# Performance work log

Measured on AMD Instinct MI355X. Metric: run time of the kernel, lower is better.

The kernel has to match this reference:

```python
import jax, jax.numpy as jnp
import numpy as np

H, HKV, D, HID = 32, 8, 128, 4096
EPS = 1e-6
ROPE_BASE = 10000.0
SCALE = D ** -0.5


def setup_inputs() -> dict:
    key = jax.random.key(0)
    ks = jax.random.split(key, 4)
    T = 2048
    x = jax.random.normal(ks[0], (T, HID), dtype=jnp.float32)
    w_qkv = jax.random.normal(ks[1], ((H + 2 * HKV) * D, HID), dtype=jnp.float32) * (HID ** -0.5)
    b_qkv = jax.random.normal(ks[2], ((H + 2 * HKV) * D,), dtype=jnp.float32) * 0.02
    q_norm_w = jnp.ones((D,), dtype=jnp.float32)
    k_norm_w = jnp.ones((D,), dtype=jnp.float32)
    w_o = jax.random.normal(ks[3], (HID, H * D), dtype=jnp.float32) * ((H * D) ** -0.5)
    return {"x": x, "w_qkv": w_qkv, "b_qkv": b_qkv, "q_norm_w": q_norm_w,
            "k_norm_w": k_norm_w, "w_o": w_o}


def _rms_norm(t, w):
    # per-head RMSNorm over the last (head_dim) axis
    var = jnp.mean(t * t, axis=-1, keepdims=True)
    return t * jax.lax.rsqrt(var + EPS) * w


def _rope(t, cos, sin):
    # neox-style half rotation; cos/sin: [T, D//2], t: [T, h, D]
    t1, t2 = jnp.split(t, 2, axis=-1)
    c = cos[:, None, :]
    s = sin[:, None, :]
    return jnp.concatenate([t1 * c - t2 * s, t2 * c + t1 * s], axis=-1)


def reference(x, w_qkv, b_qkv, q_norm_w, k_norm_w, w_o):
    T = x.shape[0]
    qkv = x @ w_qkv.T + b_qkv                      # [T, (H+2*HKV)*D]
    q, k, v = jnp.split(qkv, [H * D, (H + HKV) * D], axis=-1)
    q = q.reshape(T, H, D)
    k = k.reshape(T, HKV, D)
    v = v.reshape(T, HKV, D)

    # QK RMSNorm
    q = _rms_norm(q, q_norm_w)
    k = _rms_norm(k, k_norm_w)

    # rotary embedding, base 10000, full head_dim
    pos = jnp.arange(T, dtype=jnp.float32)
    inv_freq = 1.0 / (ROPE_BASE ** (jnp.arange(0, D, 2, dtype=jnp.float32) / D))
    freqs = pos[:, None] * inv_freq[None, :]        # [T, D//2]
    cos, sin = jnp.cos(freqs), jnp.sin(freqs)
    q = _rope(q, cos, sin)
    k = _rope(k, cos, sin)

    # GQA: kv_head_mapping = arange(HKV).repeat_interleave(H // HKV)
    groups = H // HKV
    k = jnp.repeat(k, groups, axis=1)               # [T, H, D]
    v = jnp.repeat(v, groups, axis=1)

    scores = jnp.einsum('thd,shd->hts', q, k) * SCALE   # [H, T, T]
    causal = jnp.tril(jnp.ones((T, T), dtype=bool))
    scores = jnp.where(causal[None], scores, jnp.finfo(scores.dtype).min)
    probs = jax.nn.softmax(scores, axis=-1)
    out = jnp.einsum('hts,shd->thd', probs, v)      # [T, H, D]
    return out.reshape(T, H * D) @ w_o.T            # [T, HID]
```

## Files before the change

kernel.cpp:

```cpp
#include <hip/hip_runtime.h>
#include <stdint.h>
#include <stddef.h>

typedef __bf16 bf16_t;
typedef __bf16 bf16x8 __attribute__((ext_vector_type(8)));
typedef float  f32x4  __attribute__((ext_vector_type(4)));

#define T_SEQ 2048
#define NH    32
#define NKV   8
#define DH    128
#define HIDN  4096
#define NQKV  6144
#define SCALE 0.08838834764831845f
#define MBOUND 11.5f
#define C1_EXP2 0.12751743187767f
#define C2_EXP2 16.590992970223f

__device__ inline float b2f(bf16_t v) {
  uint32_t u = ((uint32_t)__builtin_bit_cast(uint16_t, v)) << 16;
  return __builtin_bit_cast(float, u);
}
__device__ inline bf16_t f2b(float f) { return (bf16_t)f; }
__device__ inline void gl_lds16(const void* g, void* l) {
  __builtin_amdgcn_global_load_lds(
      (__attribute__((address_space(1))) void*)g,
      (__attribute__((address_space(3))) void*)l, 16, 0, 0);
}
__device__ inline f32x4 mfma16(bf16x8 a, bf16x8 b, f32x4 c) {
  return __builtin_amdgcn_mfma_f32_16x16x32_bf16(a, b, c, 0, 0, 0);
}
__device__ inline void store_val(float* p, float v)  { *p = v; }
__device__ inline void store_val(bf16_t* p, float v) { *p = f2b(v); }

__global__ __launch_bounds__(256)
void cvt2_kernel(const float* __restrict__ a, bf16_t* __restrict__ ao, int na,
                 const float* __restrict__ b, bf16_t* __restrict__ bo) {
  int blk = blockIdx.x;
  const float* in;
  bf16_t* out;
  int rb;
  if (blk < na) { in = a; out = ao; rb = blk; }
  else          { in = b; out = bo; rb = blk - na; }
  size_t i = ((size_t)rb * 256 + threadIdx.x) * 8;
  f32x4 va = *(const f32x4*)(in + i);
  f32x4 vb = *(const f32x4*)(in + i + 4);
  bf16x8 o;
#pragma unroll
  for (int e = 0; e < 4; ++e) { o[e] = f2b(va[e]); o[e + 4] = f2b(vb[e]); }
  *(bf16x8*)(out + i) = o;
}

__global__ __launch_bounds__(256)
void cvt_kernel(const float* __restrict__ in, bf16_t* __restrict__ out) {
  size_t i = ((size_t)blockIdx.x * 256 + threadIdx.x) * 8;
  f32x4 a = *(const f32x4*)(in + i);
  f32x4 b = *(const f32x4*)(in + i + 4);
  bf16x8 o;
#pragma unroll
  for (int e = 0; e < 4; ++e) { o[e] = f2b(a[e]); o[e + 4] = f2b(b[e]); }
  *(bf16x8*)(out + i) = o;
}

template <bool BIAS, typename TOUT>
__global__ __launch_bounds__(256)
void gemm_bt(const bf16_t* __restrict__ A, const bf16_t* __restrict__ Bw,
             const float* __restrict__ bias, TOUT* __restrict__ C,
             int M, int N, int K) {
  __shared__ __align__(16) char smem[32768];
  char* sA = smem;
  char* sB = smem + 16384;
  const int tid  = threadIdx.x;
  const int lane = tid & 63, wave = tid >> 6;
  const int quad = lane >> 4, l16 = lane & 15;
  const int wm = wave >> 1, wn = wave & 1;
  const int m0 = blockIdx.y * 128, n0 = blockIdx.x * 128;

  f32x4 acc[4][4] = {};
  const int kTiles = K >> 6;

  for (int kt = 0; kt < kTiles; ++kt) {
    const int kb = kt << 6;
#pragma unroll
    for (int i = 0; i < 4; ++i) {
      int p = i * 256 + tid;
      int row = p >> 3, gc = (p & 7) ^ (row & 7);
      gl_lds16(A  + (size_t)(m0 + row) * K + kb + gc * 8, sA + p * 16);
      gl_lds16(Bw + (size_t)(n0 + row) * K + kb + gc * 8, sB + p * 16);
    }
    __syncthreads();

#pragma unroll
    for (int ks = 0; ks < 2; ++ks) {
      bf16x8 af[4], bfr[4];
      const int c = ks * 4 + quad;
#pragma unroll
      for (int i = 0; i < 4; ++i) {
        int ra = wm * 64 + i * 16 + l16;
        af[i]  = *(const bf16x8*)(sA + ra * 128 + ((c ^ (ra & 7)) * 16));
        int rb = wn * 64 + i * 16 + l16;
        bfr[i] = *(const bf16x8*)(sB + rb * 128 + ((c ^ (rb & 7)) * 16));
      }
#pragma unroll
      for (int i = 0; i < 4; ++i)
#pragma unroll
        for (int j = 0; j < 4; ++j)
          acc[i][j] = mfma16(af[i], bfr[j], acc[i][j]);
    }
    __syncthreads();
  }
#pragma unroll
  for (int i = 0; i < 4; ++i) {
    int mrow = m0 + wm * 64 + i * 16 + quad * 4;
#pragma unroll
    for (int j = 0; j < 4; ++j) {
      int ncol = n0 + wn * 64 + j * 16 + l16;
      float bv = BIAS ? bias[ncol] : 0.f;
#pragma unroll
      for (int r = 0; r < 4; ++r)
        store_val(&C[(size_t)(mrow + r) * N + ncol], acc[i][j][r] + bv);
    }
  }
}

__global__ __launch_bounds__(256)
void prep_kernel(const bf16_t* __restrict__ qkv, const float* __restrict__ qw,
                 const float* __restrict__ kw, bf16_t* __restrict__ Qp,
                 bf16_t* __restrict__ Kp, bf16_t* __restrict__ Vp) {
  const int id   = blockIdx.x * 4 + (threadIdx.x >> 6);
  const int lane = threadIdx.x & 63;
  const int t = id / 48, slot = id % 48;
  const bf16_t* src = qkv + (size_t)t * NQKV + slot * DH;
  float x1 = b2f(src[lane]), x2 = b2f(src[lane + 64]);
  float o1, o2;
  if (slot < 40) {
    float ssq = x1 * x1 + x2 * x2;
#pragma unroll
    for (int m = 1; m < 64; m <<= 1) ssq += __shfl_xor(ssq, m, 64);
    float rms = rsqrtf(ssq * (1.f / 128.f) + 1e-6f);
    const float* w = (slot < 32) ? qw : kw;
    float n1 = x1 * rms * w[lane];
    float n2 = x2 * rms * w[lane + 64];
    float inv = exp2f(-0.20762050593046014f * (float)lane);
    float ang = (float)t * inv;
    float cs = __cosf(ang), sn = __sinf(ang);
    o1 = n1 * cs - n2 * sn;
    o2 = n2 * cs + n1 * sn;
  } else { o1 = x1; o2 = x2; }
  bf16_t* dst;
  if (slot < 32)      dst = Qp + ((size_t)t * NH  + slot)        * DH;
  else if (slot < 40) dst = Kp + ((size_t)t * NKV + (slot - 32)) * DH;
  else                dst = Vp + ((size_t)t * NKV + (slot - 40)) * DH;
  dst[lane] = f2b(o1); dst[lane + 64] = f2b(o2);
}

__global__ __launch_bounds__(256)
void vtrans_kernel(const bf16_t* __restrict__ Vp, bf16_t* __restrict__ Vt) {
  __shared__ bf16_t tile[64 * 66];
  const int t0 = blockIdx.x * 64, d0 = blockIdx.y * 64, kvh = blockIdx.z;
  const int tid = threadIdx.x;
#pragma unroll
  for (int i = 0; i < 2; ++i) {
    int id = i * 256 + tid;
    int tr = id >> 3, dc = id & 7;
    bf16x8 v = *(const bf16x8*)(Vp + ((size_t)(t0 + tr) * NKV + kvh) * DH + d0 + dc * 8);
#pragma unroll
    for (int e = 0; e < 8; ++e) tile[tr * 66 + dc * 8 + e] = v[e];
  }
  __syncthreads();
#pragma unroll
  for (int i = 0; i < 2; ++i) {
    int id = i * 256 + tid;
    int dr = id >> 3, tc = id & 7;
    bf16x8 o;
#pragma unroll
    for (int e = 0; e < 8; ++e) o[e] = tile[(tc * 8 + e) * 66 + dr];
    *(bf16x8*)(Vt + ((size_t)kvh * DH + d0 + dr) * T_SEQ + t0 + tc * 8) = o;
  }
}

__global__ __launch_bounds__(256)
void attn_kernel(const bf16_t* __restrict__ Qp, const bf16_t* __restrict__ Kp,
                 const bf16_t* __restrict__ Vt, bf16_t* __restrict__ Out) {
  __shared__ __align__(16) char smem[73728];
  const int tid  = threadIdx.x;
  const int lane = tid & 63, wave = tid >> 6;
  const int quad = lane >> 4, l16 = lane & 15;
  const int b = blockIdx.x, h = blockIdx.y;
  const int qt_lo = b, qt_hi = 31 - b;
  const int kvh = h >> 2;
  char* sPw = smem + 65536 + wave * 2048;

  bf16x8 qf_lo[4], qf_hi[4];
  {
    const int row_lo = qt_lo * 64 + wave * 16 + l16;
    const int row_hi = qt_hi * 64 + wave * 16 + l16;
#pragma unroll
    for (int ks = 0; ks < 4; ++ks) {
      qf_lo[ks] = *(const bf16x8*)(Qp + ((size_t)row_lo * NH + h) * DH + ks * 32 + quad * 8);
      qf_hi[ks] = *(const bf16x8*)(Qp + ((size_t)row_hi * NH + h) * DH + ks * 32 + quad * 8);
    }
  }
  f32x4 acc_lo[8] = {}, acc_hi[8] = {};
  float l_lo[4] = {0.f, 0.f, 0.f, 0.f}, l_hi[4] = {0.f, 0.f, 0.f, 0.f};

  auto stage = [&](int kt) {
    char* sK = smem + (kt & 1) * 16384;
    char* sV = smem + 32768 + (kt & 1) * 16384;
    const int k0 = kt * 64;
#pragma unroll
    for (int i = 0; i < 4; ++i) {
      int p = i * 256 + tid;
      int row = p >> 4, gc = (p & 15) ^ (row & 15);
      gl_lds16(Kp + ((size_t)(k0 + row) * NKV + kvh) * DH + gc * 8, sK + p * 16);
    }
#pragma unroll
    for (int i = 0; i < 4; ++i) {
      int p = i * 256 + tid;
      int d = p >> 3, gc = (p & 7) ^ (d & 7);
      gl_lds16(Vt + ((size_t)kvh * DH + d) * T_SEQ + k0 + gc * 8, sV + p * 16);
    }
  };

  auto compute = [&](const bf16x8 (&qf)[4], f32x4 (&acc)[8], float (&lrow)[4],
                     int qt, int kt, char* sK, char* sVT) {
    f32x4 sfr[4] = {};
    __builtin_amdgcn_s_setprio(1);
#pragma unroll
    for (int ks = 0; ks < 4; ++ks) {
      const int c = ks * 4 + quad;
#pragma unroll
      for (int j = 0; j < 4; ++j) {
        int row = j * 16 + l16;
        bf16x8 kf = *(const bf16x8*)(sK + row * 256 + ((c ^ (row & 15)) * 16));
        sfr[j] = mfma16(qf[ks], kf, sfr[j]);
      }
    }
    __builtin_amdgcn_s_setprio(0);
    float sv[4][4];
    const bool diag = (kt == qt);
#pragma unroll
    for (int j = 0; j < 4; ++j)
#pragma unroll
      for (int r = 0; r < 4; ++r) {
        float e = exp2f(fmaf(sfr[j][r], C1_EXP2, -C2_EXP2));
        if (diag) {
          int qg = wave * 16 + quad * 4 + r;
          int kg = j * 16 + l16;
          if (kg > qg) e = 0.f;
        }
        sv[j][r] = e;
      }
#pragma unroll
    for (int r = 0; r < 4; ++r)
      lrow[r] += (sv[0][r] + sv[1][r]) + (sv[2][r] + sv[3][r]);
#pragma unroll
    for (int j = 0; j < 4; ++j)
#pragma unroll
      for (int r = 0; r < 4; ++r) {
        int prow = quad * 4 + r;
        int col  = j * 16 + l16;
        int c    = col >> 3;
        ((bf16_t*)(sPw + prow * 128 + ((c ^ (prow & 7)) * 16)))[col & 7] = f2b(sv[j][r]);
      }
    __asm__ volatile("" ::: "memory");
    bf16x8 pf[2];
#pragma unroll
    for (int ks2 = 0; ks2 < 2; ++ks2) {
      int c = ks2 * 4 + quad;
      pf[ks2] = *(const bf16x8*)(sPw + l16 * 128 + ((c ^ (l16 & 7)) * 16));
    }
    __asm__ volatile("" ::: "memory");
    __builtin_amdgcn_s_setprio(1);
#pragma unroll
    for (int j2 = 0; j2 < 8; ++j2)
#pragma unroll
      for (int ks2 = 0; ks2 < 2; ++ks2) {
        int d = j2 * 16 + l16;
        int c = ks2 * 4 + quad;
        bf16x8 vf = *(const bf16x8*)(sVT + d * 128 + ((c ^ (d & 7)) * 16));
        acc[j2] = mfma16(pf[ks2], vf, acc[j2]);
      }
    __builtin_amdgcn_s_setprio(0);
  };

  stage(0);
  for (int kt = 0; kt <= qt_hi; ++kt) {
    __syncthreads();
    if (kt < qt_hi) stage(kt + 1);
    char* sK  = smem + (kt & 1) * 16384;
    char* sVT = smem + 32768 + (kt & 1) * 16384;
    compute(qf_hi, acc_hi, l_hi, qt_hi, kt, sK, sVT);
    if (kt <= qt_lo)
      compute(qf_lo, acc_lo, l_lo, qt_lo, kt, sK, sVT);
  }

#pragma unroll
  for (int r = 0; r < 4; ++r) {
    float lh = l_hi[r], ll = l_lo[r];
#pragma unroll
    for (int m = 1; m < 16; m <<= 1) {
      lh += __shfl_xor(lh, m, 64);
      ll += __shfl_xor(ll, m, 64);
    }
    float inv_h = 1.f / lh, inv_l = 1.f / ll;
    int qg_h = qt_hi * 64 + wave * 16 + quad * 4 + r;
    int qg_l = qt_lo * 64 + wave * 16 + quad * 4 + r;
#pragma unroll
    for (int j2 = 0; j2 < 8; ++j2) {
      int d = j2 * 16 + l16;
      Out[(size_t)qg_h * (NH * DH) + h * DH + d] = f2b(acc_hi[j2][r] * inv_h);
      Out[(size_t)qg_l * (NH * DH) + h * DH + d] = f2b(acc_lo[j2][r] * inv_l);
    }
  }
}

extern "C" void kernel_launch(void* const* d_in, const int* in_sizes, int n_in,
                              void* d_out, int out_size, void* d_ws, size_t ws_size,
                              hipStream_t stream) {
  const float* x    = (const float*)d_in[0];
  const float* wqkv = (const float*)d_in[1];
  const float* bqkv = (const float*)d_in[2];
  const float* qnw  = (const float*)d_in[3];
  const float* knw  = (const float*)d_in[4];
  const float* wo   = (const float*)d_in[5];
  float* out = (float*)d_out;

  char* ws = (char*)d_ws;
  bf16_t* wqkvb = (bf16_t*)(ws);
  bf16_t* xb    = (bf16_t*)(ws + 50331648);
  bf16_t* qkv   = (bf16_t*)(ws + 67108864);
  bf16_t* Qp    = (bf16_t*)(ws);
  bf16_t* Kp    = (bf16_t*)(ws + 16777216);
  bf16_t* Vp    = (bf16_t*)(ws + 20971520);
  bf16_t* Vt    = (bf16_t*)(ws + 25165824);
  bf16_t* wob   = (bf16_t*)(ws + 29360128);
  bf16_t* At    = (bf16_t*)(ws + 67108864);

  cvt2_kernel<<<16384, 256, 0, stream>>>(x, xb, 4096, wqkv, wqkvb);
  gemm_bt<true, bf16_t><<<dim3(NQKV / 128, T_SEQ / 128), 256, 0, stream>>>(
      xb, wqkvb, bqkv, qkv, T_SEQ, NQKV, HIDN);
  prep_kernel<<<(T_SEQ * 48) / 4, 256, 0, stream>>>(qkv, qnw, knw, Qp, Kp, Vp);
  vtrans_kernel<<<dim3(T_SEQ / 64, DH / 64, NKV), 256, 0, stream>>>(Vp, Vt);
  cvt_kernel<<<(HIDN * HIDN) / 2048, 256, 0, stream>>>(wo, wob);
  attn_kernel<<<dim3(16, NH), 256, 0, stream>>>(Qp, Kp, Vt, At);
  gemm_bt<false, float><<<dim3(HIDN / 128, T_SEQ / 128), 256, 0, stream>>>(
      At, wob, nullptr, out, T_SEQ, HIDN, HIDN);
}
```

Measured before the change: 533.6 us.

## Fuse QK RMSNorm, RoPE and V transpose into QKV GEMM epilogue

Adds a dedicated QKV GEMM whose epilogue stages the output tile in LDS and applies per-head RMSNorm and RoPE for Q/K slots, or writes V transposed directly. This removes the prep and vtrans kernels and the round trip of the intermediate qkv buffer through global memory. It also drops the s_setprio hints around the MFMA loops in attention and rearranges the workspace layout. The epilogue's scalar 2-byte strided stores and per-row shuffle reductions may be slower than the old vectorized paths.

```diff
diff --git a/kernel.cpp b/kernel.cpp
--- a/kernel.cpp
+++ b/kernel.cpp
@@ -13,7 +13,6 @@
 #define HIDN  4096
 #define NQKV  6144
 #define SCALE 0.08838834764831845f
-#define MBOUND 11.5f
 #define C1_EXP2 0.12751743187767f
 #define C2_EXP2 16.590992970223f
 
@@ -62,6 +61,108 @@
   *(bf16x8*)(out + i) = o;
 }
 
+__global__ __launch_bounds__(256)
+void gemm_qkv(const bf16_t* __restrict__ A, const bf16_t* __restrict__ Bw,
+              const float* __restrict__ bias, const float* __restrict__ qw,
+              const float* __restrict__ kw, bf16_t* __restrict__ Qp,
+              bf16_t* __restrict__ Kp, bf16_t* __restrict__ Vt) {
+  __shared__ __align__(16) char smem[33280];
+  char* sA = smem;
+  char* sB = smem + 16384;
+  const int tid  = threadIdx.x;
+  const int lane = tid & 63, wave = tid >> 6;
+  const int quad = lane >> 4, l16 = lane & 15;
+  const int wm = wave >> 1, wn = wave & 1;
+  const int slot = blockIdx.x;
+  const int m0 = blockIdx.y * 128, n0 = slot * 128;
+  const int K = HIDN;
+
+  f32x4 acc[4][4] = {};
+  const int kTiles = K >> 6;
+
+  for (int kt = 0; kt < kTiles; ++kt) {
+    const int kb = kt << 6;
+#pragma unroll
+    for (int i = 0; i < 4; ++i) {
+      int p = i * 256 + tid;
+      int row = p >> 3, gc = (p & 7) ^ (row & 7);
+      gl_lds16(A  + (size_t)(m0 + row) * K + kb + gc * 8, sA + p * 16);
+      gl_lds16(Bw + (size_t)(n0 + row) * K + kb + gc * 8, sB + p * 16);
+    }
+    __syncthreads();
+
+#pragma unroll
+    for (int ks = 0; ks < 2; ++ks) {
+      bf16x8 af[4], bfr[4];
+      const int c = ks * 4 + quad;
+#pragma unroll
+      for (int i = 0; i < 4; ++i) {
+        int ra = wm * 64 + i * 16 + l16;
+        af[i]  = *(const bf16x8*)(sA + ra * 128 + ((c ^ (ra & 7)) * 16));
+        int rb = wn * 64 + i * 16 + l16;
+        bfr[i] = *(const bf16x8*)(sB + rb * 128 + ((c ^ (rb & 7)) * 16));
+      }
+#pragma unroll
+      for (int i = 0; i < 4; ++i)
+#pragma unroll
+        for (int j = 0; j < 4; ++j)
+          acc[i][j] = mfma16(af[i], bfr[j], acc[i][j]);
+    }
+    __syncthreads();
+  }
+
+  bf16_t* tile = (bf16_t*)smem;
+#pragma unroll
+  for (int i = 0; i < 4; ++i) {
+    int rl = wm * 64 + i * 16 + quad * 4;
+#pragma unroll
+    for (int j = 0; j < 4; ++j) {
+      int cl = wn * 64 + j * 16 + l16;
+      float bv = bias[n0 + cl];
+#pragma unroll
+      for (int r = 0; r < 4; ++r)
+        tile[(rl + r) * 130 + cl] = f2b(acc[i][j][r] + bv);
+    }
+  }
+  __syncthreads();
+
+  if (slot < 40) {
+    const float* w = (slot < 32) ? qw : kw;
+    const float wl1 = w[lane], wl2 = w[lane + 64];
+    const float inv = exp2f(-0.20762050593046014f * (float)lane);
+    bf16_t* dstBase = (slot < 32) ? Qp + (size_t)slot * DH
+                                  : Kp + (size_t)(slot - 32) * DH;
+    const size_t dstStride = (slot < 32) ? (size_t)NH * DH : (size_t)NKV * DH;
+#pragma unroll 4
+    for (int rr = 0; rr < 32; ++rr) {
+      int row = wave * 32 + rr;
+      int t = m0 + row;
+      float x1 = b2f(tile[row * 130 + lane]);
+      float x2 = b2f(tile[row * 130 + lane + 64]);
+      float ssq = x1 * x1 + x2 * x2;
+#pragma unroll
+      for (int m = 1; m < 64; m <<= 1) ssq += __shfl_xor(ssq, m, 64);
+      float rms = rsqrtf(ssq * (1.f / 128.f) + 1e-6f);
+      float n1 = x1 * rms * wl1;
+      float n2 = x2 * rms * wl2;
+      float ang = (float)t * inv;
+      float cs = __cosf(ang), sn = __sinf(ang);
+      bf16_t* dst = dstBase + (size_t)t * dstStride;
+      dst[lane]      = f2b(n1 * cs - n2 * sn);
+      dst[lane + 64] = f2b(n2 * cs + n1 * sn);
+    }
+  } else {
+    const int kvh = slot - 40;
+#pragma unroll 4
+    for (int dd = 0; dd < 32; ++dd) {
+      int d = wave * 32 + dd;
+      bf16_t* dst = Vt + ((size_t)kvh * DH + d) * T_SEQ + m0;
+      dst[lane]      = tile[lane * 130 + d];
+      dst[lane + 64] = tile[(lane + 64) * 130 + d];
+    }
+  }
+}
+
 template <bool BIAS, typename TOUT>
 __global__ __launch_bounds__(256)
 void gemm_bt(const bf16_t* __restrict__ A, const bf16_t* __restrict__ Bw,
@@ -124,62 +225,6 @@
 }
 
 __global__ __launch_bounds__(256)
-void prep_kernel(const bf16_t* __restrict__ qkv, const float* __restrict__ qw,
-                 const float* __restrict__ kw, bf16_t* __restrict__ Qp,
-                 bf16_t* __restrict__ Kp, bf16_t* __restrict__ Vp) {
-  const int id   = blockIdx.x * 4 + (threadIdx.x >> 6);
-  const int lane = threadIdx.x & 63;
-  const int t = id / 48, slot = id % 48;
-  const bf16_t* src = qkv + (size_t)t * NQKV + slot * DH;
-  float x1 = b2f(src[lane]), x2 = b2f(src[lane + 64]);
-  float o1, o2;
-  if (slot < 40) {
-    float ssq = x1 * x1 + x2 * x2;
-#pragma unroll
-    for (int m = 1; m < 64; m <<= 1) ssq += __shfl_xor(ssq, m, 64);
-    float rms = rsqrtf(ssq * (1.f / 128.f) + 1e-6f);
-    const float* w = (slot < 32) ? qw : kw;
-    float n1 = x1 * rms * w[lane];
-    float n2 = x2 * rms * w[lane + 64];
-    float inv = exp2f(-0.20762050593046014f * (float)lane);
-    float ang = (float)t * inv;
-    float cs = __cosf(ang), sn = __sinf(ang);
-    o1 = n1 * cs - n2 * sn;
-    o2 = n2 * cs + n1 * sn;
-  } else { o1 = x1; o2 = x2; }
-  bf16_t* dst;
-  if (slot < 32)      dst = Qp + ((size_t)t * NH  + slot)        * DH;
-  else if (slot < 40) dst = Kp + ((size_t)t * NKV + (slot - 32)) * DH;
-  else                dst = Vp + ((size_t)t * NKV + (slot - 40)) * DH;
-  dst[lane] = f2b(o1); dst[lane + 64] = f2b(o2);
-}
-
-__global__ __launch_bounds__(256)
-void vtrans_kernel(const bf16_t* __restrict__ Vp, bf16_t* __restrict__ Vt) {
-  __shared__ bf16_t tile[64 * 66];
-  const int t0 = blockIdx.x * 64, d0 = blockIdx.y * 64, kvh = blockIdx.z;
-  const int tid = threadIdx.x;
-#pragma unroll
-  for (int i = 0; i < 2; ++i) {
-    int id = i * 256 + tid;
-    int tr = id >> 3, dc = id & 7;
-    bf16x8 v = *(const bf16x8*)(Vp + ((size_t)(t0 + tr) * NKV + kvh) * DH + d0 + dc * 8);
-#pragma unroll
-    for (int e = 0; e < 8; ++e) tile[tr * 66 + dc * 8 + e] = v[e];
-  }
-  __syncthreads();
-#pragma unroll
-  for (int i = 0; i < 2; ++i) {
-    int id = i * 256 + tid;
-    int dr = id >> 3, tc = id & 7;
-    bf16x8 o;
-#pragma unroll
-    for (int e = 0; e < 8; ++e) o[e] = tile[(tc * 8 + e) * 66 + dr];
-    *(bf16x8*)(Vt + ((size_t)kvh * DH + d0 + dr) * T_SEQ + t0 + tc * 8) = o;
-  }
-}
-
-__global__ __launch_bounds__(256)
 void attn_kernel(const bf16_t* __restrict__ Qp, const bf16_t* __restrict__ Kp,
                  const bf16_t* __restrict__ Vt, bf16_t* __restrict__ Out) {
   __shared__ __align__(16) char smem[73728];
@@ -225,7 +270,6 @@
   auto compute = [&](const bf16x8 (&qf)[4], f32x4 (&acc)[8], float (&lrow)[4],
                      int qt, int kt, char* sK, char* sVT) {
     f32x4 sfr[4] = {};
-    __builtin_amdgcn_s_setprio(1);
 #pragma unroll
     for (int ks = 0; ks < 4; ++ks) {
       const int c = ks * 4 + quad;
@@ -236,7 +280,6 @@
         sfr[j] = mfma16(qf[ks], kf, sfr[j]);
       }
     }
-    __builtin_amdgcn_s_setprio(0);
     float sv[4][4];
     const bool diag = (kt == qt);
 #pragma unroll
@@ -271,7 +314,6 @@
       pf[ks2] = *(const bf16x8*)(sPw + l16 * 128 + ((c ^ (l16 & 7)) * 16));
     }
     __asm__ volatile("" ::: "memory");
-    __builtin_amdgcn_s_setprio(1);
 #pragma unroll
     for (int j2 = 0; j2 < 8; ++j2)
 #pragma unroll
@@ -281,7 +323,6 @@
         bf16x8 vf = *(const bf16x8*)(sVT + d * 128 + ((c ^ (d & 7)) * 16));
         acc[j2] = mfma16(pf[ks2], vf, acc[j2]);
       }
-    __builtin_amdgcn_s_setprio(0);
   };
 
   stage(0);
@@ -329,19 +370,15 @@
   char* ws = (char*)d_ws;
   bf16_t* wqkvb = (bf16_t*)(ws);
   bf16_t* xb    = (bf16_t*)(ws + 50331648);
-  bf16_t* qkv   = (bf16_t*)(ws + 67108864);
-  bf16_t* Qp    = (bf16_t*)(ws);
-  bf16_t* Kp    = (bf16_t*)(ws + 16777216);
-  bf16_t* Vp    = (bf16_t*)(ws + 20971520);
-  bf16_t* Vt    = (bf16_t*)(ws + 25165824);
-  bf16_t* wob   = (bf16_t*)(ws + 29360128);
-  bf16_t* At    = (bf16_t*)(ws + 67108864);
+  bf16_t* Qp    = (bf16_t*)(ws + 67108864);
+  bf16_t* Kp    = (bf16_t*)(ws + 83886080);
+  bf16_t* Vt    = (bf16_t*)(ws + 88080384);
+  bf16_t* wob   = (bf16_t*)(ws);
+  bf16_t* At    = (bf16_t*)(ws + 33554432);
 
   cvt2_kernel<<<16384, 256, 0, stream>>>(x, xb, 4096, wqkv, wqkvb);
-  gemm_bt<true, bf16_t><<<dim3(NQKV / 128, T_SEQ / 128), 256, 0, stream>>>(
-      xb, wqkvb, bqkv, qkv, T_SEQ, NQKV, HIDN);
-  prep_kernel<<<(T_SEQ * 48) / 4, 256, 0, stream>>>(qkv, qnw, knw, Qp, Kp, Vp);
-  vtrans_kernel<<<dim3(T_SEQ / 64, DH / 64, NKV), 256, 0, stream>>>(Vp, Vt);
+  gemm_qkv<<<dim3(NQKV / 128, T_SEQ / 128), 256, 0, stream>>>(
+      xb, wqkvb, bqkv, qnw, knw, Qp, Kp, Vt);
   cvt_kernel<<<(HIDN * HIDN) / 2048, 256, 0, stream>>>(wo, wob);
   attn_kernel<<<dim3(16, NH), 256, 0, stream>>>(Qp, Kp, Vt, At);
   gemm_bt<false, float><<<dim3(HIDN / 128, T_SEQ / 128), 256, 0, stream>>>(
```

Result: slower. 550.9 us (+3.2%).

## Fuse QK prep, V transpose and w_o conversion into one postproc kernel

Applied to the files above, without the earlier changes.

Merges three small kernels into a single launch that splits work by block index: QK RMSNorm+RoPE, V transpose read directly from the qkv buffer, and the w_o fp32-to-bf16 conversion. This removes the intermediate Vp buffer and its extra write and read pass, and saves two kernel launches. It also drops the s_setprio hints around the MFMA loops in the attention kernel, which may change wave scheduling. The shared-memory tile is now allocated for every block, including those that do not use it.

```diff
diff --git a/kernel.cpp b/kernel.cpp
--- a/kernel.cpp
+++ b/kernel.cpp
@@ -13,7 +13,6 @@
 #define HIDN  4096
 #define NQKV  6144
 #define SCALE 0.08838834764831845f
-#define MBOUND 11.5f
 #define C1_EXP2 0.12751743187767f
 #define C2_EXP2 16.590992970223f
 
@@ -51,17 +50,6 @@
   *(bf16x8*)(out + i) = o;
 }
 
-__global__ __launch_bounds__(256)
-void cvt_kernel(const float* __restrict__ in, bf16_t* __restrict__ out) {
-  size_t i = ((size_t)blockIdx.x * 256 + threadIdx.x) * 8;
-  f32x4 a = *(const f32x4*)(in + i);
-  f32x4 b = *(const f32x4*)(in + i + 4);
-  bf16x8 o;
-#pragma unroll
-  for (int e = 0; e < 4; ++e) { o[e] = f2b(a[e]); o[e + 4] = f2b(b[e]); }
-  *(bf16x8*)(out + i) = o;
-}
-
 template <bool BIAS, typename TOUT>
 __global__ __launch_bounds__(256)
 void gemm_bt(const bf16_t* __restrict__ A, const bf16_t* __restrict__ Bw,
@@ -123,17 +111,25 @@
   }
 }
 
+#define PP_PREP_BLOCKS 20480
+#define PP_VT_BLOCKS   512
+#define PP_CVT_BLOCKS  8192
 __global__ __launch_bounds__(256)
-void prep_kernel(const bf16_t* __restrict__ qkv, const float* __restrict__ qw,
-                 const float* __restrict__ kw, bf16_t* __restrict__ Qp,
-                 bf16_t* __restrict__ Kp, bf16_t* __restrict__ Vp) {
-  const int id   = blockIdx.x * 4 + (threadIdx.x >> 6);
-  const int lane = threadIdx.x & 63;
-  const int t = id / 48, slot = id % 48;
-  const bf16_t* src = qkv + (size_t)t * NQKV + slot * DH;
-  float x1 = b2f(src[lane]), x2 = b2f(src[lane + 64]);
-  float o1, o2;
-  if (slot < 40) {
+void postproc_kernel(const bf16_t* __restrict__ qkv,
+                     const float* __restrict__ qw, const float* __restrict__ kw,
+                     const float* __restrict__ wo,
+                     bf16_t* __restrict__ Qp, bf16_t* __restrict__ Kp,
+                     bf16_t* __restrict__ Vt, bf16_t* __restrict__ wob) {
+  __shared__ bf16_t tile[64 * 66];
+  const int bid = blockIdx.x;
+  const int tid = threadIdx.x;
+
+  if (bid < PP_PREP_BLOCKS) {
+    const int id   = bid * 4 + (tid >> 6);
+    const int lane = tid & 63;
+    const int t = id / 40, slot = id % 40;
+    const bf16_t* src = qkv + (size_t)t * NQKV + slot * DH;
+    float x1 = b2f(src[lane]), x2 = b2f(src[lane + 64]);
     float ssq = x1 * x1 + x2 * x2;
 #pragma unroll
     for (int m = 1; m < 64; m <<= 1) ssq += __shfl_xor(ssq, m, 64);
@@ -144,38 +140,41 @@
     float inv = exp2f(-0.20762050593046014f * (float)lane);
     float ang = (float)t * inv;
     float cs = __cosf(ang), sn = __sinf(ang);
-    o1 = n1 * cs - n2 * sn;
-    o2 = n2 * cs + n1 * sn;
-  } else { o1 = x1; o2 = x2; }
-  bf16_t* dst;
-  if (slot < 32)      dst = Qp + ((size_t)t * NH  + slot)        * DH;
-  else if (slot < 40) dst = Kp + ((size_t)t * NKV + (slot - 32)) * DH;
-  else                dst = Vp + ((size_t)t * NKV + (slot - 40)) * DH;
-  dst[lane] = f2b(o1); dst[lane + 64] = f2b(o2);
-}
-
-__global__ __launch_bounds__(256)
-void vtrans_kernel(const bf16_t* __restrict__ Vp, bf16_t* __restrict__ Vt) {
-  __shared__ bf16_t tile[64 * 66];
-  const int t0 = blockIdx.x * 64, d0 = blockIdx.y * 64, kvh = blockIdx.z;
-  const int tid = threadIdx.x;
-#pragma unroll
-  for (int i = 0; i < 2; ++i) {
-    int id = i * 256 + tid;
-    int tr = id >> 3, dc = id & 7;
-    bf16x8 v = *(const bf16x8*)(Vp + ((size_t)(t0 + tr) * NKV + kvh) * DH + d0 + dc * 8);
-#pragma unroll
-    for (int e = 0; e < 8; ++e) tile[tr * 66 + dc * 8 + e] = v[e];
-  }
-  __syncthreads();
-#pragma unroll
-  for (int i = 0; i < 2; ++i) {
-    int id = i * 256 + tid;
-    int dr = id >> 3, tc = id & 7;
+    bf16_t* dst = (slot < 32) ? Qp + ((size_t)t * NH  + slot)        * DH
+                              : Kp + ((size_t)t * NKV + (slot - 32)) * DH;
+    dst[lane]      = f2b(n1 * cs - n2 * sn);
+    dst[lane + 64] = f2b(n2 * cs + n1 * sn);
+  } else if (bid < PP_PREP_BLOCKS + PP_VT_BLOCKS) {
+    const int b = bid - PP_PREP_BLOCKS;
+    const int t0 = (b & 31) * 64, d0 = ((b >> 5) & 1) * 64, kvh = b >> 6;
+#pragma unroll
+    for (int i = 0; i < 2; ++i) {
+      int id = i * 256 + tid;
+      int tr = id >> 3, dc = id & 7;
+      bf16x8 v = *(const bf16x8*)(qkv + (size_t)(t0 + tr) * NQKV +
+                                  (40 + kvh) * DH + d0 + dc * 8);
+#pragma unroll
+      for (int e = 0; e < 8; ++e) tile[tr * 66 + dc * 8 + e] = v[e];
+    }
+    __syncthreads();
+#pragma unroll
+    for (int i = 0; i < 2; ++i) {
+      int id = i * 256 + tid;
+      int dr = id >> 3, tc = id & 7;
+      bf16x8 o;
+#pragma unroll
+      for (int e = 0; e < 8; ++e) o[e] = tile[(tc * 8 + e) * 66 + dr];
+      *(bf16x8*)(Vt + ((size_t)kvh * DH + d0 + dr) * T_SEQ + t0 + tc * 8) = o;
+    }
+  } else {
+    const int c = bid - (PP_PREP_BLOCKS + PP_VT_BLOCKS);
+    size_t i = ((size_t)c * 256 + tid) * 8;
+    f32x4 a = *(const f32x4*)(wo + i);
+    f32x4 bq = *(const f32x4*)(wo + i + 4);
     bf16x8 o;
 #pragma unroll
-    for (int e = 0; e < 8; ++e) o[e] = tile[(tc * 8 + e) * 66 + dr];
-    *(bf16x8*)(Vt + ((size_t)kvh * DH + d0 + dr) * T_SEQ + t0 + tc * 8) = o;
+    for (int e = 0; e < 4; ++e) { o[e] = f2b(a[e]); o[e + 4] = f2b(bq[e]); }
+    *(bf16x8*)(wob + i) = o;
   }
 }
 
@@ -225,7 +224,6 @@
   auto compute = [&](const bf16x8 (&qf)[4], f32x4 (&acc)[8], float (&lrow)[4],
                      int qt, int kt, char* sK, char* sVT) {
     f32x4 sfr[4] = {};
-    __builtin_amdgcn_s_setprio(1);
 #pragma unroll
     for (int ks = 0; ks < 4; ++ks) {
       const int c = ks * 4 + quad;
@@ -236,7 +234,6 @@
         sfr[j] = mfma16(qf[ks], kf, sfr[j]);
       }
     }
-    __builtin_amdgcn_s_setprio(0);
     float sv[4][4];
     const bool diag = (kt == qt);
 #pragma unroll
@@ -271,7 +268,6 @@
       pf[ks2] = *(const bf16x8*)(sPw + l16 * 128 + ((c ^ (l16 & 7)) * 16));
     }
     __asm__ volatile("" ::: "memory");
-    __builtin_amdgcn_s_setprio(1);
 #pragma unroll
     for (int j2 = 0; j2 < 8; ++j2)
 #pragma unroll
@@ -281,7 +277,6 @@
         bf16x8 vf = *(const bf16x8*)(sVT + d * 128 + ((c ^ (d & 7)) * 16));
         acc[j2] = mfma16(pf[ks2], vf, acc[j2]);
       }
-    __builtin_amdgcn_s_setprio(0);
   };
 
   stage(0);
@@ -332,17 +327,15 @@
   bf16_t* qkv   = (bf16_t*)(ws + 67108864);
   bf16_t* Qp    = (bf16_t*)(ws);
   bf16_t* Kp    = (bf16_t*)(ws + 16777216);
-  bf16_t* Vp    = (bf16_t*)(ws + 20971520);
-  bf16_t* Vt    = (bf16_t*)(ws + 25165824);
-  bf16_t* wob   = (bf16_t*)(ws + 29360128);
+  bf16_t* Vt    = (bf16_t*)(ws + 20971520);
+  bf16_t* wob   = (bf16_t*)(ws + 25165824);
   bf16_t* At    = (bf16_t*)(ws + 67108864);
 
   cvt2_kernel<<<16384, 256, 0, stream>>>(x, xb, 4096, wqkv, wqkvb);
   gemm_bt<true, bf16_t><<<dim3(NQKV / 128, T_SEQ / 128), 256, 0, stream>>>(
       xb, wqkvb, bqkv, qkv, T_SEQ, NQKV, HIDN);
-  prep_kernel<<<(T_SEQ * 48) / 4, 256, 0, stream>>>(qkv, qnw, knw, Qp, Kp, Vp);
-  vtrans_kernel<<<dim3(T_SEQ / 64, DH / 64, NKV), 256, 0, stream>>>(Vp, Vt);
-  cvt_kernel<<<(HIDN * HIDN) / 2048, 256, 0, stream>>>(wo, wob);
+  postproc_kernel<<<PP_PREP_BLOCKS + PP_VT_BLOCKS + PP_CVT_BLOCKS, 256, 0, stream>>>(
+      qkv, qnw, knw, wo, Qp, Kp, Vt, wob);
   attn_kernel<<<dim3(16, NH), 256, 0, stream>>>(Qp, Kp, Vt, At);
   gemm_bt<false, float><<<dim3(HIDN / 128, T_SEQ / 128), 256, 0, stream>>>(
       At, wob, nullptr, out, T_SEQ, HIDN, HIDN);
```

Result: slower. 553.8 us (+3.8%).
